# Kernel optimization log

Measured on AMD Instinct MI355X. Metric: run time of the kernel, lower is better.

The kernel has to match this reference:

```python
import jax, jax.numpy as jnp
import numpy as np

IN_FEATURES = 4096
OUT_FEATURES = 4096
RANK = 16
TOKENS = 8192


def setup_inputs() -> dict:
    key = jax.random.key(0)
    k1, k2, k3, k4, k5 = jax.random.split(key, 5)
    x = jax.random.normal(k1, (TOKENS, IN_FEATURES), dtype=jnp.float32)
    orig_weight = jax.random.normal(k2, (IN_FEATURES, OUT_FEATURES), dtype=jnp.float32) * 0.02
    lora_u = jax.random.normal(k3, (IN_FEATURES, RANK), dtype=jnp.float32) * 0.02
    lora_s = jax.random.uniform(k4, (RANK,), dtype=jnp.float32)
    lora_vt = jax.random.normal(k5, (RANK, OUT_FEATURES), dtype=jnp.float32) * 0.02
    return {"x": x, "orig_weight": orig_weight, "lora_u": lora_u,
            "lora_s": lora_s, "lora_vt": lora_vt}


def reference(x, orig_weight, lora_u, lora_s, lora_vt):
    # Faithful to torch: W = orig_weight + lora_u @ diag(lora_s) @ lora_vt; out = x @ W
    # diag(s) contraction expressed as a column scale of lora_u (same math).
    delta = (lora_u * lora_s[None, :]) @ lora_vt  # [in, out] low-rank delta
    return x @ (orig_weight + delta)
```

## Files before the change

### kernel.cpp

```cpp
#include <hip/hip_runtime.h>
#include <hip/hip_bf16.h>
#include <stdint.h>

#define TOKENS 8192
#define NF 4096
#define KF 4096
#define RANK 16

typedef __attribute__((ext_vector_type(8))) short bf16x8;
typedef __attribute__((ext_vector_type(4))) float f32x4;
typedef __attribute__((ext_vector_type(8))) unsigned short u16x8;

static __device__ __forceinline__ unsigned short f2b(float f) {
    union { float f; uint32_t u; } v; v.f = f;
    uint32_t u = v.u;
    uint32_t r = (u + 0x7fffu + ((u >> 16) & 1u)) >> 16;
    return (unsigned short)r;
}

__global__ __launch_bounds__(256) void prep_w_kernel(
    const float* __restrict__ W, const float* __restrict__ U,
    const float* __restrict__ s, const float* __restrict__ Vt,
    unsigned short* __restrict__ Wt)
{
    __shared__ float Us[64][16];
    __shared__ float Vs[16][64];
    __shared__ float tile[64][65];
    const int kb = blockIdx.x, nb = blockIdx.y;
    const int t = threadIdx.x;
    for (int idx = t; idx < 64 * 16; idx += 256) {
        int kl = idx >> 4, r = idx & 15;
        Us[kl][r] = U[(size_t)(kb * 64 + kl) * RANK + r];
    }
    for (int idx = t; idx < 16 * 64; idx += 256) {
        int r = idx >> 6, nl = idx & 63;
        Vs[r][nl] = Vt[(size_t)r * NF + nb * 64 + nl] * s[r];
    }
    __syncthreads();
    const int nl = t & 63, kl0 = t >> 6;
    for (int i = 0; i < 16; ++i) {
        int kl = kl0 + i * 4;
        float v = __builtin_nontemporal_load(&W[(size_t)(kb * 64 + kl) * NF + nb * 64 + nl]);
        #pragma unroll
        for (int r = 0; r < RANK; ++r) v += Us[kl][r] * Vs[r][nl];
        tile[kl][nl] = v;
    }
    __syncthreads();
    #pragma unroll
    for (int j = 0; j < 2; ++j) {
        int idx = t + j * 256;
        int kg = idx & 7, n = idx >> 3;
        u16x8 o;
        #pragma unroll
        for (int e = 0; e < 8; ++e) o[e] = f2b(tile[kg * 8 + e][n]);
        *(u16x8*)&Wt[(size_t)(nb * 64 + n) * KF + kb * 64 + kg * 8] = o;
    }
}

__global__ __launch_bounds__(256) void prep_x_kernel(
    const float* __restrict__ x, unsigned short* __restrict__ xb)
{
    size_t base = ((size_t)blockIdx.x * 256 + threadIdx.x) * 8;
    f32x4 a = __builtin_nontemporal_load((const f32x4*)(x + base));
    f32x4 b = __builtin_nontemporal_load((const f32x4*)(x + base + 4));
    u16x8 o;
    o[0] = f2b(a[0]); o[1] = f2b(a[1]); o[2] = f2b(a[2]); o[3] = f2b(a[3]);
    o[4] = f2b(b[0]); o[5] = f2b(b[1]); o[6] = f2b(b[2]); o[7] = f2b(b[3]);
    *(u16x8*)(xb + base) = o;
}


#define VM4  asm volatile("s_waitcnt vmcnt(4)" ::: "memory")
#define NOVM

#define PHASE(d, q, bfr, STAGE_EXPR, VMW) do {                                  \
    bf16x8 af0k0 = ldA(d, 2*(q), 0),   af0k1 = ldA(d, 2*(q), 1);                \
    bf16x8 af1k0 = ldA(d, 2*(q)+1, 0), af1k1 = ldA(d, 2*(q)+1, 1);              \
    STAGE_EXPR;                                                                 \
    VMW;                                                                        \
    __builtin_amdgcn_s_barrier();                                               \
    asm volatile("s_waitcnt lgkmcnt(0)" ::: "memory");                          \
    __builtin_amdgcn_s_setprio(1);                                              \
    _Pragma("unroll")                                                           \
    for (int nf = 0; nf < 4; ++nf) {                                            \
        acc[2*(q)][nf]   = __builtin_amdgcn_mfma_f32_16x16x32_bf16(af0k0, bfr[nf][0], acc[2*(q)][nf],   0,0,0); \
        acc[2*(q)][nf]   = __builtin_amdgcn_mfma_f32_16x16x32_bf16(af0k1, bfr[nf][1], acc[2*(q)][nf],   0,0,0); \
        acc[2*(q)+1][nf] = __builtin_amdgcn_mfma_f32_16x16x32_bf16(af1k0, bfr[nf][0], acc[2*(q)+1][nf], 0,0,0); \
        acc[2*(q)+1][nf] = __builtin_amdgcn_mfma_f32_16x16x32_bf16(af1k1, bfr[nf][1], acc[2*(q)+1][nf], 0,0,0); \
    }                                                                           \
    __builtin_amdgcn_s_setprio(0);                                              \
    __builtin_amdgcn_s_barrier();                                               \
} while (0)

#define LDB_ALL(d, bfr) do {                                                    \
    _Pragma("unroll")                                                           \
    for (int nf = 0; nf < 4; ++nf) {                                            \
        bfr[nf][0] = ldB(d, nf, 0);                                             \
        bfr[nf][1] = ldB(d, nf, 1);                                             \
    } } while (0)

__global__ __launch_bounds__(512, 2) void gemm_kernel(
    const unsigned short* __restrict__ A,
    const unsigned short* __restrict__ Bt,
    float* __restrict__ C)
{
    __shared__ __align__(16) unsigned short lds[65536];

    const int tid  = threadIdx.x;
    const int lane = tid & 63;
    const int wave = tid >> 6;
    const int wm = wave >> 2;
    const int wn = wave & 3;

    const int bid = blockIdx.x;
    const int swz = (bid & 7) * 64 + (bid >> 3);
    const int tm = swz >> 4;
    const int tn = swz & 15;

    const int frow = lane & 15;
    const int kgrp = lane >> 4;
    const int xorv = (frow & 7) << 4;

    const int st_row  = tid >> 3;
    const int st_colE = ((((tid & 7) * 16) ^ (((tid >> 3) & 7) << 4)) >> 1);
    const unsigned short* aSrc = A  + (size_t)(tm * 256 + st_row) * KF + st_colE;
    const unsigned short* bSrc = Bt + (size_t)(tn * 256 + st_row) * KF + st_colE;
    const int dstE = tid * 8;

    f32x4 acc[8][4] = {};

    auto stage = [&](int isB, int d, int h, int kt) {
        const unsigned short* src =
            (isB ? bSrc : aSrc) + (size_t)((h) * 128) * KF + (kt) * 64;
        unsigned short* dst = (unsigned short*)&lds[isB * 32768 + (d * 2 + h) * 8192 + dstE];
        __builtin_amdgcn_global_load_lds(
            (const __attribute__((address_space(1))) void*)src,
            (__attribute__((address_space(3))) void*)dst, 16, 0, 0);
        __builtin_amdgcn_global_load_lds(
            (const __attribute__((address_space(1))) void*)(src + (size_t)64 * KF),
            (__attribute__((address_space(3))) void*)(dst + 4096), 16, 0, 0);
    };

    auto ldA = [&](int d, int mf, int kk) -> bf16x8 {
        int off = (d * 2 + wm) * 8192 + (mf * 16 + frow) * 64
                + ((((kk << 6) | (kgrp << 4)) ^ xorv) >> 1);
        return *(const bf16x8*)&lds[off];
    };
    auto ldB = [&](int d, int nf, int kk) -> bf16x8 {
        int off = 32768 + (d * 2 + (wn >> 1)) * 8192
                + ((wn & 1) * 64 + nf * 16 + frow) * 64
                + ((((kk << 6) | (kgrp << 4)) ^ xorv) >> 1);
        return *(const bf16x8*)&lds[off];
    };

    stage(1, 0, 0, 0); stage(1, 0, 1, 0);
    stage(0, 0, 0, 0); stage(0, 0, 1, 0);
    stage(1, 1, 0, 1); stage(1, 1, 1, 1);
    VM4;
    __builtin_amdgcn_s_barrier();

    for (int i = 0; i < 32; ++i) {
        const int kt1 = 2 * i + 1;
        const int kt2 = (2 * i + 2) & 63;
        const int kt3 = (2 * i + 3) & 63;

        bf16x8 bfr[4][2];
        LDB_ALL(0, bfr);
        PHASE(0, 0, bfr, (stage(0, 1, 0, kt1), stage(0, 1, 1, kt1)), NOVM);
        PHASE(0, 1, bfr, stage(1, 0, 0, kt2), NOVM);
        PHASE(0, 2, bfr, stage(1, 0, 1, kt2), NOVM);
        PHASE(0, 3, bfr, (void)0, VM4);
        LDB_ALL(1, bfr);
        PHASE(1, 0, bfr, stage(0, 0, 0, kt2), NOVM);
        PHASE(1, 1, bfr, (stage(0, 0, 1, kt2), stage(1, 1, 0, kt3)), NOVM);
        PHASE(1, 2, bfr, stage(1, 1, 1, kt3), NOVM);
        PHASE(1, 3, bfr, (void)0, VM4);
    }

    asm volatile("s_waitcnt vmcnt(0)" ::: "memory");

    const int rgrp = lane >> 4, coll = lane & 15;
    #pragma unroll
    for (int mf = 0; mf < 8; ++mf)
        #pragma unroll
        for (int nf = 0; nf < 4; ++nf) {
            size_t row0 = (size_t)(tm * 256 + wm * 128 + mf * 16 + rgrp * 4);
            size_t col  = (size_t)(tn * 256 + wn * 64 + nf * 16 + coll);
            #pragma unroll
            for (int r = 0; r < 4; ++r)
                __builtin_nontemporal_store(acc[mf][nf][r], &C[(row0 + r) * NF + col]);
        }
}

extern "C" void kernel_launch(void* const* d_in, const int* in_sizes, int n_in,
                              void* d_out, int out_size, void* d_ws, size_t ws_size,
                              hipStream_t stream) {
    const float* x  = (const float*)d_in[0];
    const float* W  = (const float*)d_in[1];
    const float* U  = (const float*)d_in[2];
    const float* s  = (const float*)d_in[3];
    const float* Vt = (const float*)d_in[4];
    float* out = (float*)d_out;

    unsigned short* Wt = (unsigned short*)d_ws;
    unsigned short* xb = Wt + (size_t)NF * KF;

    prep_w_kernel<<<dim3(KF / 64, NF / 64), 256, 0, stream>>>(W, U, s, Vt, Wt);
    prep_x_kernel<<<(TOKENS * KF / 8) / 256, 256, 0, stream>>>(x, xb);
    gemm_kernel<<<(TOKENS / 256) * (NF / 256), 512, 0, stream>>>(xb, Wt, out);
}
```

Measured before the change: 305.3 us.

## Switch GEMM inner loop to 32x32x16 bf16 MFMA with rebalanced staging

Replaces the 16x16x32 MFMA tiles with 32x32x16 MFMAs. Each wave now holds 4x2 accumulators of 16 floats instead of 8x4 of 4, and the LDS fragment addressing and output store mapping are changed to match. The global-to-LDS staging is redistributed so each phase issues one stage call, and the output stores are no longer nontemporal. The larger MFMA shape is meant to cut fragment LDS reads per FLOP and instruction issue overhead, at the cost of a new LDS access pattern that may hit bank conflicts under the existing XOR swizzle.

```diff
diff --git a/kernel.cpp b/kernel.cpp
--- a/kernel.cpp
+++ b/kernel.cpp
@@ -9,6 +9,7 @@
 
 typedef __attribute__((ext_vector_type(8))) short bf16x8;
 typedef __attribute__((ext_vector_type(4))) float f32x4;
+typedef __attribute__((ext_vector_type(16))) float f32x16;
 typedef __attribute__((ext_vector_type(8))) unsigned short u16x8;
 
 static __device__ __forceinline__ unsigned short f2b(float f) {
@@ -74,19 +75,19 @@
 #define NOVM
 
 #define PHASE(d, q, bfr, STAGE_EXPR, VMW) do {                                  \
-    bf16x8 af0k0 = ldA(d, 2*(q), 0),   af0k1 = ldA(d, 2*(q), 1);                \
-    bf16x8 af1k0 = ldA(d, 2*(q)+1, 0), af1k1 = ldA(d, 2*(q)+1, 1);              \
+    bf16x8 af0 = ldA(d, q, 0), af1 = ldA(d, q, 1);                              \
+    bf16x8 af2 = ldA(d, q, 2), af3 = ldA(d, q, 3);                              \
     STAGE_EXPR;                                                                 \
     VMW;                                                                        \
     __builtin_amdgcn_s_barrier();                                               \
     asm volatile("s_waitcnt lgkmcnt(0)" ::: "memory");                          \
     __builtin_amdgcn_s_setprio(1);                                              \
     _Pragma("unroll")                                                           \
-    for (int nf = 0; nf < 4; ++nf) {                                            \
-        acc[2*(q)][nf]   = __builtin_amdgcn_mfma_f32_16x16x32_bf16(af0k0, bfr[nf][0], acc[2*(q)][nf],   0,0,0); \
-        acc[2*(q)][nf]   = __builtin_amdgcn_mfma_f32_16x16x32_bf16(af0k1, bfr[nf][1], acc[2*(q)][nf],   0,0,0); \
-        acc[2*(q)+1][nf] = __builtin_amdgcn_mfma_f32_16x16x32_bf16(af1k0, bfr[nf][0], acc[2*(q)+1][nf], 0,0,0); \
-        acc[2*(q)+1][nf] = __builtin_amdgcn_mfma_f32_16x16x32_bf16(af1k1, bfr[nf][1], acc[2*(q)+1][nf], 0,0,0); \
+    for (int nf = 0; nf < 2; ++nf) {                                            \
+        acc[q][nf] = __builtin_amdgcn_mfma_f32_32x32x16_bf16(af0, bfr[nf][0], acc[q][nf], 0,0,0); \
+        acc[q][nf] = __builtin_amdgcn_mfma_f32_32x32x16_bf16(af1, bfr[nf][1], acc[q][nf], 0,0,0); \
+        acc[q][nf] = __builtin_amdgcn_mfma_f32_32x32x16_bf16(af2, bfr[nf][2], acc[q][nf], 0,0,0); \
+        acc[q][nf] = __builtin_amdgcn_mfma_f32_32x32x16_bf16(af3, bfr[nf][3], acc[q][nf], 0,0,0); \
     }                                                                           \
     __builtin_amdgcn_s_setprio(0);                                              \
     __builtin_amdgcn_s_barrier();                                               \
@@ -94,10 +95,11 @@
 
 #define LDB_ALL(d, bfr) do {                                                    \
     _Pragma("unroll")                                                           \
-    for (int nf = 0; nf < 4; ++nf) {                                            \
-        bfr[nf][0] = ldB(d, nf, 0);                                             \
-        bfr[nf][1] = ldB(d, nf, 1);                                             \
-    } } while (0)
+    for (int nf = 0; nf < 2; ++nf)                                              \
+        _Pragma("unroll")                                                       \
+        for (int ks = 0; ks < 4; ++ks)                                          \
+            bfr[nf][ks] = ldB(d, nf, ks);                                       \
+    } while (0)
 
 __global__ __launch_bounds__(512, 2) void gemm_kernel(
     const unsigned short* __restrict__ A,
@@ -117,9 +119,9 @@
     const int tm = swz >> 4;
     const int tn = swz & 15;
 
-    const int frow = lane & 15;
-    const int kgrp = lane >> 4;
-    const int xorv = (frow & 7) << 4;
+    const int l31 = lane & 31;
+    const int khalf = lane >> 5;
+    const int xorv = (l31 & 7) << 4;
 
     const int st_row  = tid >> 3;
     const int st_colE = ((((tid & 7) * 16) ^ (((tid >> 3) & 7) << 4)) >> 1);
@@ -127,7 +129,7 @@
     const unsigned short* bSrc = Bt + (size_t)(tn * 256 + st_row) * KF + st_colE;
     const int dstE = tid * 8;
 
-    f32x4 acc[8][4] = {};
+    f32x16 acc[4][2] = {};
 
     auto stage = [&](int isB, int d, int h, int kt) {
         const unsigned short* src =
@@ -141,15 +143,16 @@
             (__attribute__((address_space(3))) void*)(dst + 4096), 16, 0, 0);
     };
 
-    auto ldA = [&](int d, int mf, int kk) -> bf16x8 {
-        int off = (d * 2 + wm) * 8192 + (mf * 16 + frow) * 64
-                + ((((kk << 6) | (kgrp << 4)) ^ xorv) >> 1);
+    auto ldA = [&](int d, int q, int ks) -> bf16x8 {
+        int row = q * 32 + l31;
+        int cb  = (ks * 32 + khalf * 16) ^ xorv;
+        int off = (d * 2 + wm) * 8192 + row * 64 + (cb >> 1);
         return *(const bf16x8*)&lds[off];
     };
-    auto ldB = [&](int d, int nf, int kk) -> bf16x8 {
-        int off = 32768 + (d * 2 + (wn >> 1)) * 8192
-                + ((wn & 1) * 64 + nf * 16 + frow) * 64
-                + ((((kk << 6) | (kgrp << 4)) ^ xorv) >> 1);
+    auto ldB = [&](int d, int nf, int ks) -> bf16x8 {
+        int nrow = (wn & 1) * 64 + nf * 32 + l31;
+        int cb   = (ks * 32 + khalf * 16) ^ xorv;
+        int off  = 32768 + (d * 2 + (wn >> 1)) * 8192 + nrow * 64 + (cb >> 1);
         return *(const bf16x8*)&lds[off];
     };
 
@@ -164,31 +167,32 @@
         const int kt2 = (2 * i + 2) & 63;
         const int kt3 = (2 * i + 3) & 63;
 
-        bf16x8 bfr[4][2];
+        bf16x8 bfr[2][4];
         LDB_ALL(0, bfr);
-        PHASE(0, 0, bfr, (stage(0, 1, 0, kt1), stage(0, 1, 1, kt1)), NOVM);
-        PHASE(0, 1, bfr, stage(1, 0, 0, kt2), NOVM);
-        PHASE(0, 2, bfr, stage(1, 0, 1, kt2), NOVM);
-        PHASE(0, 3, bfr, (void)0, VM4);
+        PHASE(0, 0, bfr, stage(0, 1, 0, kt1), NOVM);
+        PHASE(0, 1, bfr, stage(0, 1, 1, kt1), NOVM);
+        PHASE(0, 2, bfr, stage(1, 0, 0, kt2), NOVM);
+        PHASE(0, 3, bfr, stage(1, 0, 1, kt2), VM4);
         LDB_ALL(1, bfr);
         PHASE(1, 0, bfr, stage(0, 0, 0, kt2), NOVM);
-        PHASE(1, 1, bfr, (stage(0, 0, 1, kt2), stage(1, 1, 0, kt3)), NOVM);
-        PHASE(1, 2, bfr, stage(1, 1, 1, kt3), NOVM);
-        PHASE(1, 3, bfr, (void)0, VM4);
+        PHASE(1, 1, bfr, stage(0, 0, 1, kt2), NOVM);
+        PHASE(1, 2, bfr, stage(1, 1, 0, kt3), NOVM);
+        PHASE(1, 3, bfr, stage(1, 1, 1, kt3), VM4);
     }
 
     asm volatile("s_waitcnt vmcnt(0)" ::: "memory");
 
-    const int rgrp = lane >> 4, coll = lane & 15;
     #pragma unroll
-    for (int mf = 0; mf < 8; ++mf)
+    for (int q = 0; q < 4; ++q)
         #pragma unroll
-        for (int nf = 0; nf < 4; ++nf) {
-            size_t row0 = (size_t)(tm * 256 + wm * 128 + mf * 16 + rgrp * 4);
-            size_t col  = (size_t)(tn * 256 + wn * 64 + nf * 16 + coll);
+        for (int nf = 0; nf < 2; ++nf) {
+            size_t col   = (size_t)(tn * 256 + wn * 64 + nf * 32 + l31);
+            int    rbase = tm * 256 + wm * 128 + q * 32 + khalf * 4;
             #pragma unroll
-            for (int r = 0; r < 4; ++r)
-                __builtin_nontemporal_store(acc[mf][nf][r], &C[(row0 + r) * NF + col]);
+            for (int r = 0; r < 16; ++r) {
+                int row = rbase + (r & 3) + 8 * (r >> 2);
+                C[(size_t)row * NF + col] = acc[q][nf][r];
+            }
         }
 }
 
```

Result: slower. 326.8 us (+7.0%).

## Double-buffer B fragments and prefetch next half-tile during MFMA phase

Applied to the files above, without the earlier changes.

B-fragment register loads for the next LDS buffer are issued inside the last MFMA phase of each half-iteration, using two register sets (P/Q) so the LDS reads overlap with matrix math instead of stalling at the start of each half. Global-to-LDS staging is also respread one stage per phase, and the output stores change from nontemporal to regular stores. The cost is higher VGPR pressure from two B-fragment buffers at 2 waves/SIMD occupancy, plus a risk of LDS hazards if the new wait placement is off.

```diff
diff --git a/kernel.cpp b/kernel.cpp
--- a/kernel.cpp
+++ b/kernel.cpp
@@ -71,26 +71,15 @@
 
 
 #define VM4  asm volatile("s_waitcnt vmcnt(4)" ::: "memory")
-#define NOVM
-
-#define PHASE(d, q, bfr, STAGE_EXPR, VMW) do {                                  \
-    bf16x8 af0k0 = ldA(d, 2*(q), 0),   af0k1 = ldA(d, 2*(q), 1);                \
-    bf16x8 af1k0 = ldA(d, 2*(q)+1, 0), af1k1 = ldA(d, 2*(q)+1, 1);              \
-    STAGE_EXPR;                                                                 \
-    VMW;                                                                        \
-    __builtin_amdgcn_s_barrier();                                               \
-    asm volatile("s_waitcnt lgkmcnt(0)" ::: "memory");                          \
-    __builtin_amdgcn_s_setprio(1);                                              \
+
+#define MFMA16(q, bfr) do {                                                     \
     _Pragma("unroll")                                                           \
     for (int nf = 0; nf < 4; ++nf) {                                            \
         acc[2*(q)][nf]   = __builtin_amdgcn_mfma_f32_16x16x32_bf16(af0k0, bfr[nf][0], acc[2*(q)][nf],   0,0,0); \
         acc[2*(q)][nf]   = __builtin_amdgcn_mfma_f32_16x16x32_bf16(af0k1, bfr[nf][1], acc[2*(q)][nf],   0,0,0); \
         acc[2*(q)+1][nf] = __builtin_amdgcn_mfma_f32_16x16x32_bf16(af1k0, bfr[nf][0], acc[2*(q)+1][nf], 0,0,0); \
         acc[2*(q)+1][nf] = __builtin_amdgcn_mfma_f32_16x16x32_bf16(af1k1, bfr[nf][1], acc[2*(q)+1][nf], 0,0,0); \
-    }                                                                           \
-    __builtin_amdgcn_s_setprio(0);                                              \
-    __builtin_amdgcn_s_barrier();                                               \
-} while (0)
+    } } while (0)
 
 #define LDB_ALL(d, bfr) do {                                                    \
     _Pragma("unroll")                                                           \
@@ -98,6 +87,32 @@
         bfr[nf][0] = ldB(d, nf, 0);                                             \
         bfr[nf][1] = ldB(d, nf, 1);                                             \
     } } while (0)
+
+#define PHASE(d, q, bfr, STAGE_EXPR) do {                                       \
+    bf16x8 af0k0 = ldA(d, 2*(q), 0),   af0k1 = ldA(d, 2*(q), 1);                \
+    bf16x8 af1k0 = ldA(d, 2*(q)+1, 0), af1k1 = ldA(d, 2*(q)+1, 1);              \
+    STAGE_EXPR;                                                                 \
+    __builtin_amdgcn_s_barrier();                                               \
+    asm volatile("s_waitcnt lgkmcnt(0)" ::: "memory");                          \
+    __builtin_amdgcn_s_setprio(1);                                              \
+    MFMA16(q, bfr);                                                             \
+    __builtin_amdgcn_s_setprio(0);                                              \
+    __builtin_amdgcn_s_barrier();                                               \
+} while (0)
+
+#define PHASEX(d, q, bfr, bnxt, dnxt, STAGE_EXPR) do {                          \
+    bf16x8 af0k0 = ldA(d, 2*(q), 0),   af0k1 = ldA(d, 2*(q), 1);                \
+    bf16x8 af1k0 = ldA(d, 2*(q)+1, 0), af1k1 = ldA(d, 2*(q)+1, 1);              \
+    STAGE_EXPR;                                                                 \
+    VM4;                                                                        \
+    __builtin_amdgcn_s_barrier();                                               \
+    asm volatile("s_waitcnt lgkmcnt(0)" ::: "memory");                          \
+    __builtin_amdgcn_s_setprio(1);                                              \
+    LDB_ALL(dnxt, bnxt);                                                        \
+    MFMA16(q, bfr);                                                             \
+    __builtin_amdgcn_s_setprio(0);                                              \
+    __builtin_amdgcn_s_barrier();                                               \
+} while (0)
 
 __global__ __launch_bounds__(512, 2) void gemm_kernel(
     const unsigned short* __restrict__ A,
@@ -153,28 +168,29 @@
         return *(const bf16x8*)&lds[off];
     };
 
+    bf16x8 bfrP[4][2], bfrQ[4][2];
+
     stage(1, 0, 0, 0); stage(1, 0, 1, 0);
     stage(0, 0, 0, 0); stage(0, 0, 1, 0);
     stage(1, 1, 0, 1); stage(1, 1, 1, 1);
     VM4;
     __builtin_amdgcn_s_barrier();
+    asm volatile("" ::: "memory");
+    LDB_ALL(0, bfrP);
 
     for (int i = 0; i < 32; ++i) {
         const int kt1 = 2 * i + 1;
         const int kt2 = (2 * i + 2) & 63;
         const int kt3 = (2 * i + 3) & 63;
 
-        bf16x8 bfr[4][2];
-        LDB_ALL(0, bfr);
-        PHASE(0, 0, bfr, (stage(0, 1, 0, kt1), stage(0, 1, 1, kt1)), NOVM);
-        PHASE(0, 1, bfr, stage(1, 0, 0, kt2), NOVM);
-        PHASE(0, 2, bfr, stage(1, 0, 1, kt2), NOVM);
-        PHASE(0, 3, bfr, (void)0, VM4);
-        LDB_ALL(1, bfr);
-        PHASE(1, 0, bfr, stage(0, 0, 0, kt2), NOVM);
-        PHASE(1, 1, bfr, (stage(0, 0, 1, kt2), stage(1, 1, 0, kt3)), NOVM);
-        PHASE(1, 2, bfr, stage(1, 1, 1, kt3), NOVM);
-        PHASE(1, 3, bfr, (void)0, VM4);
+        PHASE (0, 0, bfrP, stage(0, 1, 0, kt1));
+        PHASE (0, 1, bfrP, stage(0, 1, 1, kt1));
+        PHASE (0, 2, bfrP, stage(1, 0, 0, kt2));
+        PHASEX(0, 3, bfrP, bfrQ, 1, stage(1, 0, 1, kt2));
+        PHASE (1, 0, bfrQ, stage(0, 0, 0, kt2));
+        PHASE (1, 1, bfrQ, stage(0, 0, 1, kt2));
+        PHASE (1, 2, bfrQ, stage(1, 1, 0, kt3));
+        PHASEX(1, 3, bfrQ, bfrP, 0, stage(1, 1, 1, kt3));
     }
 
     asm volatile("s_waitcnt vmcnt(0)" ::: "memory");
@@ -188,7 +204,7 @@
             size_t col  = (size_t)(tn * 256 + wn * 64 + nf * 16 + coll);
             #pragma unroll
             for (int r = 0; r < 4; ++r)
-                __builtin_nontemporal_store(acc[mf][nf][r], &C[(row0 + r) * NF + col]);
+                C[(row0 + r) * NF + col] = acc[mf][nf][r];
         }
 }
 
```

After: 289.3 us. 1.06x faster.
